# Performance work log

Hardware: AMD Instinct MI355X
Metric: run time of the kernel (lower is better)

## Reference

```python
import jax, jax.numpy as jnp
import numpy as np

N_NODES = 50000
N_EDGES = 800000
SIZES = [128, 256, 256, 128]
EPS = 1e-5


def setup_inputs() -> dict:
    key = jax.random.key(0)
    ks = jax.random.split(key, 2 + 5 * (len(SIZES) - 1))
    inp = {
        "x": jax.random.normal(ks[0], (N_NODES, SIZES[0]), dtype=jnp.float32),
        "edge_index": jax.random.randint(ks[1], (2, N_EDGES), 0, N_NODES, dtype=jnp.int64),
    }
    k = 2
    for i, (fin, fout) in enumerate(zip(SIZES[:-1], SIZES[1:])):
        scale = 1.0 / np.sqrt(fin)
        inp[f"W{i}"] = jax.random.normal(ks[k], (fout, fin), dtype=jnp.float32) * scale; k += 1
        inp[f"b{i}"] = jnp.zeros((fout,), dtype=jnp.float32)
        inp[f"g{i}"] = jnp.ones((fout,), dtype=jnp.float32)   # LayerNorm weight
        inp[f"be{i}"] = jnp.zeros((fout,), dtype=jnp.float32)  # LayerNorm bias
        inp[f"a{i}"] = jnp.full((1,), 0.25, dtype=jnp.float32)  # PReLU slope
        k += 3  # keep key consumption deterministic
    return inp


def _gcn_conv(x, src, dst, dinv, W, b):
    # GCNConv: h = x @ W^T; aggregate norm(src,dst) * h[src] into dst; add bias.
    h = x @ W.T  # [N, F_out]
    norm = dinv[src] * dinv[dst]  # [E+N]
    msg = norm[:, None] * h[src]  # [E+N, F_out]
    return jax.ops.segment_sum(msg, dst, num_segments=N_NODES) + b


def _layernorm_graph(x, g, be):
    # PyG LayerNorm(mode='graph'): normalize over all nodes and channels.
    mu = x.mean()
    xc = x - mu
    var = (xc * xc).mean()
    return xc / jnp.sqrt(var + EPS) * g + be


def _prelu(x, a):
    return jnp.where(x >= 0, x, a * x)


def reference(x, edge_index, W0, b0, g0, be0, a0, W1, b1, g1, be1, a1, W2, b2, g2, be2, a2):
    loop = jnp.arange(N_NODES, dtype=edge_index.dtype)
    src = jnp.concatenate([edge_index[0], loop])  # add self-loops
    dst = jnp.concatenate([edge_index[1], loop])
    deg = jax.ops.segment_sum(jnp.ones_like(dst, dtype=x.dtype), dst, num_segments=N_NODES)
    dinv = jax.lax.rsqrt(deg)  # deg >= 1 due to self-loops
    params = [(W0, b0, g0, be0, a0), (W1, b1, g1, be1, a1), (W2, b2, g2, be2, a2)]
    for W, b, g, be, a in params:
        x = _gcn_conv(x, src, dst, dinv, W, b)
        x = _layernorm_graph(x, g, be)
        x = _prelu(x, a)
    return x
```

## Files before the change

kernel.cpp:

```cpp
#include <hip/hip_runtime.h>

#define N_NODES 50000
#define N_EDGES 800000
#define EPS 1e-5f

typedef __attribute__((ext_vector_type(8))) short bf16x8;
typedef __attribute__((ext_vector_type(4))) float f32x4;
typedef __attribute__((ext_vector_type(4))) unsigned short us4;

__device__ __forceinline__ unsigned short f2b(float f) {
    union { float f; unsigned int u; } v; v.f = f;
    unsigned int r = v.u + 0x7fffu + ((v.u >> 16) & 1u);
    return (unsigned short)(r >> 16);
}
__device__ __forceinline__ float b2f(unsigned short b) {
    union { unsigned int u; float f; } v; v.u = ((unsigned int)b) << 16;
    return v.f;
}

#define RED_BUCKETS 64
#define RED_FLOATS_PER_LAYER (RED_BUCKETS * 16)


#define CV_NX (N_NODES * 128 / 4)
#define CV_N0 (256 * 128 / 4)
#define CV_N1 (256 * 256 / 4)
#define CV_N2 (128 * 256 / 4)

__global__ void prep_kernel(const float* __restrict__ x0, const float* __restrict__ W0,
                            const float* __restrict__ W1, const float* __restrict__ W2,
                            unsigned short* __restrict__ xb, unsigned short* __restrict__ wb0,
                            unsigned short* __restrict__ wb1, unsigned short* __restrict__ wb2,
                            int* __restrict__ deg, int* __restrict__ fill,
                            float* __restrict__ red) {
    int i = blockIdx.x * 256 + threadIdx.x;
    if (i < N_NODES) { deg[i] = 0; fill[i] = 0; }
    if (i < 3 * RED_FLOATS_PER_LAYER) red[i] = 0.f;
    const float* s;
    unsigned short* d;
    int j = i;
    if (j < CV_NX) { s = x0; d = xb; }
    else if ((j -= CV_NX) < CV_N0) { s = W0; d = wb0; }
    else if ((j -= CV_N0) < CV_N1) { s = W1; d = wb1; }
    else if ((j -= CV_N1) < CV_N2) { s = W2; d = wb2; }
    else return;
    float4 v = reinterpret_cast<const float4*>(s)[j];
    us4 o;
    o[0] = f2b(v.x); o[1] = f2b(v.y); o[2] = f2b(v.z); o[3] = f2b(v.w);
    reinterpret_cast<us4*>(d)[j] = o;
}


__global__ void count_kernel(const int* __restrict__ dst, int* __restrict__ deg, int e) {
    for (int i = blockIdx.x * blockDim.x + threadIdx.x; i < e; i += gridDim.x * blockDim.x)
        atomicAdd(&deg[dst[i]], 1);
}

__global__ void scan1_kernel(const int* __restrict__ deg, float* __restrict__ dinv,
                             int* __restrict__ bsum, int n) {
    int i = blockIdx.x * 256 + threadIdx.x;
    int v = (i < n) ? deg[i] : 0;
    if (i < n) dinv[i] = rsqrtf((float)(v + 1));
    int t = v;
    #pragma unroll
    for (int off = 1; off < 64; off <<= 1) t += __shfl_xor(t, off);
    __shared__ int wsum[4];
    int wid = threadIdx.x >> 6, lane = threadIdx.x & 63;
    if (lane == 0) wsum[wid] = t;
    __syncthreads();
    if (threadIdx.x == 0) bsum[blockIdx.x] = wsum[0] + wsum[1] + wsum[2] + wsum[3];
}

__global__ void scan2_kernel(const int* __restrict__ bsum, int* __restrict__ bpre, int nb) {
    __shared__ int sm[256];
    int t = threadIdx.x;
    sm[t] = (t < nb) ? bsum[t] : 0;
    __syncthreads();
    #pragma unroll
    for (int d = 1; d < 256; d <<= 1) {
        int x = (t >= d) ? sm[t - d] : 0;
        __syncthreads();
        sm[t] += x;
        __syncthreads();
    }
    bpre[t] = (t > 0) ? sm[t - 1] : 0;
}

__global__ void scan3_kernel(const int* __restrict__ deg, const int* __restrict__ bpre,
                             int* __restrict__ off, int n) {
    __shared__ int sm[256];
    int t = threadIdx.x;
    int i = blockIdx.x * 256 + t;
    int v = (i < n) ? deg[i] : 0;
    sm[t] = v;
    __syncthreads();
    #pragma unroll
    for (int d = 1; d < 256; d <<= 1) {
        int x = (t >= d) ? sm[t - d] : 0;
        __syncthreads();
        sm[t] += x;
        __syncthreads();
    }
    if (i < n) off[i + 1] = sm[t] + bpre[blockIdx.x];
    if (i == 0) off[0] = 0;
}

__global__ void scatter_kernel(const int* __restrict__ src, const int* __restrict__ dst,
                               const int* __restrict__ coff, int* __restrict__ fill,
                               const float* __restrict__ dinv,
                               unsigned int* __restrict__ epack, int e) {
    for (int i = blockIdx.x * blockDim.x + threadIdx.x; i < e; i += gridDim.x * blockDim.x) {
        int d = dst[i];
        int s = src[i];
        int pos = coff[d] + atomicAdd(&fill[d], 1);
        epack[pos] = ((unsigned int)f2b(dinv[s] * dinv[d]) << 16) | (unsigned int)s;
    }
}


template<int BN, bool TRANSFORM, bool ADD_BIAS, bool FUSE_RED>
__device__ __forceinline__ void gemm_body(
    const unsigned short* __restrict__ Xin, const unsigned short* __restrict__ Wb,
    const float* __restrict__ bias, const float* __restrict__ redin,
    const float* __restrict__ gw, const float* __restrict__ bw,
    const float* __restrict__ asl, float* __restrict__ redout,
    unsigned short* __restrict__ Hout, int M, int K, float inv_count) {
    constexpr int FR_N = BN / 64;
    __shared__ unsigned short xs[2][64 * 32];
    int tid = threadIdx.x;
    int wid = tid >> 6, lane = tid & 63;
    int l16 = lane & 15, kg = lane >> 4;
    int srow = tid >> 2, sblk = tid & 3;
    int m0 = blockIdx.x * 64;
    int colbase = wid * (BN / 4);

    float mu = 0.f, rstd = 0.f, alpha = 0.f;
    if (TRANSFORM) {
        float s = redin[lane * 16], s2 = redin[lane * 16 + 1];
        #pragma unroll
        for (int off = 1; off < 64; off <<= 1) { s += __shfl_xor(s, off); s2 += __shfl_xor(s2, off); }
        mu = s * inv_count;
        rstd = rsqrtf(s2 * inv_count - mu * mu + EPS);
        alpha = asl[0];
    }

    int gm = m0 + srow;
    bool inm = (gm < M);
    const unsigned short* xrow = Xin + (size_t)gm * K + sblk * 8;
    unsigned short* xdst = &xs[0][srow * 32 + ((sblk ^ (srow & 3)) * 8)];

    auto stage = [&](int k0, int buf) {
        bf16x8 xv = {};
        if (inm) {
            bf16x8 u = *reinterpret_cast<const bf16x8*>(xrow + k0);
            if (TRANSFORM) {
                int f0 = k0 + sblk * 8;
                float ga[8], ba[8];
                *reinterpret_cast<float4*>(&ga[0]) = *reinterpret_cast<const float4*>(gw + f0);
                *reinterpret_cast<float4*>(&ga[4]) = *reinterpret_cast<const float4*>(gw + f0 + 4);
                *reinterpret_cast<float4*>(&ba[0]) = *reinterpret_cast<const float4*>(bw + f0);
                *reinterpret_cast<float4*>(&ba[4]) = *reinterpret_cast<const float4*>(bw + f0 + 4);
                #pragma unroll
                for (int i = 0; i < 8; ++i) {
                    float A = rstd * ga[i];
                    float B = ba[i] - mu * A;
                    float v = fmaf(b2f((unsigned short)u[i]), A, B);
                    v = fmaf(fminf(v, 0.f), alpha - 1.0f, v);
                    xv[i] = (short)f2b(v);
                }
            } else {
                xv = u;
            }
        }
        *reinterpret_cast<bf16x8*>(xdst + buf * (64 * 32)) = xv;
    };

    stage(0, 0);
    f32x4 acc[4][FR_N] = {};
    int nsteps = K / 32;
    for (int s = 0; s < nsteps; ++s) {
        __syncthreads();
        int k0 = s * 32;
        if (s + 1 < nsteps) stage(k0 + 32, (s + 1) & 1);
        bf16x8 b[FR_N];
        #pragma unroll
        for (int j = 0; j < FR_N; ++j)
            b[j] = *reinterpret_cast<const bf16x8*>(
                Wb + (size_t)(colbase + j * 16 + l16) * K + k0 + kg * 8);
        const unsigned short* xbuf = xs[s & 1];
        bf16x8 a[4];
        #pragma unroll
        for (int i = 0; i < 4; ++i) {
            int ar = i * 16 + l16;
            a[i] = *reinterpret_cast<const bf16x8*>(xbuf + ar * 32 + ((kg ^ (ar & 3)) * 8));
        }
        #pragma unroll
        for (int i = 0; i < 4; ++i)
            #pragma unroll
            for (int j = 0; j < FR_N; ++j)
                acc[i][j] = __builtin_amdgcn_mfma_f32_16x16x32_bf16(b[j], a[i], acc[i][j], 0, 0, 0);
    }

    float bsel[FR_N][4];
    if (ADD_BIAS) {
        #pragma unroll
        for (int j = 0; j < FR_N; ++j)
            *reinterpret_cast<float4*>(bsel[j]) =
                *reinterpret_cast<const float4*>(bias + colbase + j * 16 + kg * 4);
    }
    float s = 0.f, s2 = 0.f;
    #pragma unroll
    for (int i = 0; i < 4; ++i) {
        int row = m0 + i * 16 + l16;
        if (row < M) {
            #pragma unroll
            for (int j = 0; j < FR_N; ++j) {
                us4 o;
                #pragma unroll
                for (int r = 0; r < 4; ++r) {
                    float v = acc[i][j][r] + (ADD_BIAS ? bsel[j][r] : 0.f);
                    if (FUSE_RED) { s += v; s2 += v * v; }
                    o[r] = f2b(v);
                }
                *reinterpret_cast<us4*>(Hout + (size_t)row * BN + colbase + j * 16 + kg * 4) = o;
            }
        }
    }
    if (FUSE_RED) {
        #pragma unroll
        for (int off = 1; off < 64; off <<= 1) { s += __shfl_xor(s, off); s2 += __shfl_xor(s2, off); }
        if (lane == 0) {
            int bkt = (blockIdx.x & (RED_BUCKETS - 1)) * 16;
            atomicAdd(&redout[bkt], s);
            atomicAdd(&redout[bkt + 1], s2);
        }
    }
}


template<int COLS, bool ADD_BIAS, bool FUSE_RED>
__device__ __forceinline__ void agg_body(
    const unsigned short* __restrict__ Hb, const int* __restrict__ coff,
    const unsigned int* __restrict__ epack, const float* __restrict__ dinv,
    const float* __restrict__ bias, unsigned short* __restrict__ Y,
    float* __restrict__ red) {
    constexpr int RL = COLS / 8;
    constexpr int NG = 64 / RL;
    int node = blockIdx.x * 4 + (threadIdx.x >> 6);
    int lane = threadIdx.x & 63;
    int g = lane / RL;
    int rl = lane % RL;
    float di = dinv[node];
    int s0 = coff[node], s1 = coff[node + 1];
    float acc[8] = {};

    int k = s0 - 1 + g;
    int sc; float wc;
    bf16x8 vc;
    bool have = (k < s1);
    if (have) {
        if (k < s0) { sc = node; wc = di * di; }
        else { unsigned int u = epack[k]; sc = u & 0xffff; wc = b2f((unsigned short)(u >> 16)); }
        vc = *reinterpret_cast<const bf16x8*>(Hb + (size_t)sc * COLS + rl * 8);
    }
    while (have) {
        int k2 = k + NG;
        bool have2 = (k2 < s1);
        int sn = 0; float wn = 0.f;
        bf16x8 vn;
        if (have2) {
            unsigned int u = epack[k2];
            sn = u & 0xffff; wn = b2f((unsigned short)(u >> 16));
            vn = *reinterpret_cast<const bf16x8*>(Hb + (size_t)sn * COLS + rl * 8);
        }
        #pragma unroll
        for (int i = 0; i < 8; ++i) acc[i] += wc * b2f((unsigned short)vc[i]);
        k = k2; wc = wn; vc = vn; have = have2;
    }

    #pragma unroll
    for (int off = RL; off < 64; off <<= 1) {
        #pragma unroll
        for (int i = 0; i < 8; ++i) acc[i] += __shfl_xor(acc[i], off);
    }
    if (ADD_BIAS) {
        #pragma unroll
        for (int i = 0; i < 8; ++i) acc[i] += bias[rl * 8 + i];
    }
    if (FUSE_RED) {
        float s = 0.f, s2 = 0.f;
        if (g == 0) {
            #pragma unroll
            for (int i = 0; i < 8; ++i) { s += acc[i]; s2 += acc[i] * acc[i]; }
        }
        #pragma unroll
        for (int off = 1; off < 64; off <<= 1) { s += __shfl_xor(s, off); s2 += __shfl_xor(s2, off); }
        if (lane == 0) {
            int bkt = (blockIdx.x & (RED_BUCKETS - 1)) * 16;
            atomicAdd(&red[bkt], s);
            atomicAdd(&red[bkt + 1], s2);
        }
    }
    if (g == 0) {
        bf16x8 o;
        #pragma unroll
        for (int i = 0; i < 8; ++i) o[i] = (short)f2b(acc[i]);
        __builtin_nontemporal_store(o, reinterpret_cast<bf16x8*>(Y + (size_t)node * COLS + rl * 8));
    }
}


__global__ __launch_bounds__(256) void gemm_l0(const unsigned short* X, const unsigned short* W,
                                               const float* bias, float* redout,
                                               unsigned short* H, int M, int K, float ic) {
    gemm_body<256, false, true, true>(X, W, bias, nullptr, nullptr, nullptr, nullptr, redout, H, M, K, ic);
}
__global__ __launch_bounds__(256) void gemm_l1(const unsigned short* X, const unsigned short* W,
                                               const float* redin, const float* gw, const float* bw,
                                               const float* asl, unsigned short* H, int M, int K, float ic) {
    gemm_body<256, true, false, false>(X, W, nullptr, redin, gw, bw, asl, nullptr, H, M, K, ic);
}
__global__ __launch_bounds__(256) void gemm_l2(const unsigned short* X, const unsigned short* W,
                                               const float* redin, const float* gw, const float* bw,
                                               const float* asl, unsigned short* H, int M, int K, float ic) {
    gemm_body<128, true, false, false>(X, W, nullptr, redin, gw, bw, asl, nullptr, H, M, K, ic);
}
__global__ void agg_l0(const unsigned short* Hb, const int* coff, const unsigned int* ep,
                       const float* dinv, unsigned short* Y) {
    agg_body<128, false, false>(Hb, coff, ep, dinv, nullptr, Y, nullptr);
}
__global__ void agg_l1(const unsigned short* Hb, const int* coff, const unsigned int* ep,
                       const float* dinv, const float* bias, unsigned short* Y, float* red) {
    agg_body<256, true, true>(Hb, coff, ep, dinv, bias, Y, red);
}
__global__ void agg_l2(const unsigned short* Hb, const int* coff, const unsigned int* ep,
                       const float* dinv, const float* bias, unsigned short* Y, float* red) {
    agg_body<128, true, true>(Hb, coff, ep, dinv, bias, Y, red);
}


__global__ void norm_final(const unsigned short* __restrict__ Yb, const float* __restrict__ red,
                           const float* __restrict__ g, const float* __restrict__ be,
                           const float* __restrict__ a, float* __restrict__ X,
                           int fmask8, int n8, float inv_count) {
    int lane = threadIdx.x & 63;
    float s = red[lane * 16], s2 = red[lane * 16 + 1];
    #pragma unroll
    for (int off = 1; off < 64; off <<= 1) { s += __shfl_xor(s, off); s2 += __shfl_xor(s2, off); }
    float mu = s * inv_count;
    float rstd = rsqrtf(s2 * inv_count - mu * mu + EPS);
    float alpha = a[0];
    for (int i = blockIdx.x * blockDim.x + threadIdx.x; i < n8; i += gridDim.x * blockDim.x) {
        bf16x8 v = reinterpret_cast<const bf16x8*>(Yb)[i];
        int fb = (i & fmask8) * 8;
        float o[8];
        #pragma unroll
        for (int j = 0; j < 8; ++j) {
            float t = (b2f((unsigned short)v[j]) - mu) * rstd * g[fb + j] + be[fb + j];
            o[j] = t >= 0.f ? t : alpha * t;
        }
        float* xp = X + (size_t)i * 8;
        *reinterpret_cast<float4*>(xp) = make_float4(o[0], o[1], o[2], o[3]);
        *reinterpret_cast<float4*>(xp + 4) = make_float4(o[4], o[5], o[6], o[7]);
    }
}


extern "C" void kernel_launch(void* const* d_in, const int* in_sizes, int n_in,
                              void* d_out, int out_size, void* d_ws, size_t ws_size,
                              hipStream_t stream) {
    const float* x0 = (const float*)d_in[0];
    const int* ei = (const int*)d_in[1];
    const float* W[3] = {(const float*)d_in[2], (const float*)d_in[7], (const float*)d_in[12]};
    const float* bb[3] = {(const float*)d_in[3], (const float*)d_in[8], (const float*)d_in[13]};
    const float* gg[3] = {(const float*)d_in[4], (const float*)d_in[9], (const float*)d_in[14]};
    const float* be[3] = {(const float*)d_in[5], (const float*)d_in[10], (const float*)d_in[15]};
    const float* aa[3] = {(const float*)d_in[6], (const float*)d_in[11], (const float*)d_in[16]};

    char* ws = (char*)d_ws;
    size_t o = 0;
    auto alloc = [&](size_t bytes) {
        void* p = ws + o;
        o = (o + bytes + 255) & ~(size_t)255;
        return p;
    };
    int* deg = (int*)alloc(N_NODES * 4);
    int* fill = (int*)alloc(N_NODES * 4);
    int* coff = (int*)alloc((N_NODES + 1) * 4);
    unsigned int* epack = (unsigned int*)alloc((size_t)N_EDGES * 4);
    float* dinv = (float*)alloc(N_NODES * 4);
    int* bsum = (int*)alloc(256 * 4);
    int* bpre = (int*)alloc(256 * 4);
    float* red = (float*)alloc(3 * RED_FLOATS_PER_LAYER * 4);
    unsigned short* Wb0 = (unsigned short*)alloc(256 * 128 * 2);
    unsigned short* Wb1 = (unsigned short*)alloc(256 * 256 * 2);
    unsigned short* Wb2 = (unsigned short*)alloc(128 * 256 * 2);
    unsigned short* xb = (unsigned short*)alloc((size_t)N_NODES * 128 * 2);
    unsigned short* hb = (unsigned short*)alloc((size_t)N_NODES * 256 * 2);
    unsigned short* yb = (unsigned short*)alloc((size_t)N_NODES * 256 * 2);

    const int* e_src = ei;
    const int* e_dst = ei + N_EDGES;
    int nb = (N_NODES + 255) / 256;

    int cvtot = CV_NX + CV_N0 + CV_N1 + CV_N2;
    prep_kernel<<<(cvtot + 255) / 256, 256, 0, stream>>>(x0, W[0], W[1], W[2], xb, Wb0, Wb1, Wb2,
                                                         deg, fill, red);
    count_kernel<<<2048, 256, 0, stream>>>(e_dst, deg, N_EDGES);
    scan1_kernel<<<nb, 256, 0, stream>>>(deg, dinv, bsum, N_NODES);
    scan2_kernel<<<1, 256, 0, stream>>>(bsum, bpre, nb);
    scan3_kernel<<<nb, 256, 0, stream>>>(deg, bpre, coff, N_NODES);
    scatter_kernel<<<2048, 256, 0, stream>>>(e_src, e_dst, coff, fill, dinv, epack, N_EDGES);

    int gm = (N_NODES + 63) / 64;
    float ic256 = 1.0f / (N_NODES * 256.0f);
    float ic128 = 1.0f / (N_NODES * 128.0f);

    agg_l0<<<12500, 256, 0, stream>>>(xb, coff, epack, dinv, hb);
    gemm_l0<<<gm, 256, 0, stream>>>(hb, Wb0, bb[0], red + 0, yb, N_NODES, 128, ic256);

    gemm_l1<<<gm, 256, 0, stream>>>(yb, Wb1, red + 0, gg[0], be[0], aa[0], hb, N_NODES, 256, ic256);
    agg_l1<<<12500, 256, 0, stream>>>(hb, coff, epack, dinv, bb[1], yb, red + RED_FLOATS_PER_LAYER);

    gemm_l2<<<gm, 256, 0, stream>>>(yb, Wb2, red + RED_FLOATS_PER_LAYER, gg[1], be[1], aa[1], hb,
                                    N_NODES, 256, ic256);
    agg_l2<<<12500, 256, 0, stream>>>(hb, coff, epack, dinv, bb[2], yb,
                                      red + 2 * RED_FLOATS_PER_LAYER);

    norm_final<<<2048, 256, 0, stream>>>(yb, red + 2 * RED_FLOATS_PER_LAYER, gg[2], be[2], aa[2],
                                         (float*)d_out, 15, N_NODES * 128 / 8, ic128);
}
```

Measured before the change: 341.1 us.

## Store node features in 32-column chunked layout and aggregate per chunk

Node feature buffers now use a column-chunked layout: each 32-feature slice of all nodes is stored contiguously, so one gathered row segment is 64 bytes. The aggregation kernel changes to match. Each block handles one chunk for 64 nodes, and each node's edge list is walked serially by 4 lanes, with no cross-lane shuffle reduction. The intent is a smaller gather working set per chunk, for better L2 hit rates on the random neighbor reads. In exchange, load balancing across lanes now depends on node degree, and the GEMM and final-normalisation kernels need extra index arithmetic and strided stores.

```diff
diff --git a/kernel.cpp b/kernel.cpp
--- a/kernel.cpp
+++ b/kernel.cpp
@@ -17,6 +17,7 @@
     union { unsigned int u; float f; } v; v.u = ((unsigned int)b) << 16;
     return v.f;
 }
+
 
 #define RED_BUCKETS 64
 #define RED_FLOATS_PER_LAYER (RED_BUCKETS * 16)
@@ -36,11 +37,19 @@
     int i = blockIdx.x * 256 + threadIdx.x;
     if (i < N_NODES) { deg[i] = 0; fill[i] = 0; }
     if (i < 3 * RED_FLOATS_PER_LAYER) red[i] = 0.f;
+    int j = i;
+    if (j < CV_NX) {
+        float4 v = reinterpret_cast<const float4*>(x0)[j];
+        int n = j >> 5;
+        int col0 = (j & 31) * 4;
+        us4 o;
+        o[0] = f2b(v.x); o[1] = f2b(v.y); o[2] = f2b(v.z); o[3] = f2b(v.w);
+        *reinterpret_cast<us4*>(xb + ((size_t)(col0 >> 5) * N_NODES + n) * 32 + (col0 & 31)) = o;
+        return;
+    }
     const float* s;
     unsigned short* d;
-    int j = i;
-    if (j < CV_NX) { s = x0; d = xb; }
-    else if ((j -= CV_NX) < CV_N0) { s = W0; d = wb0; }
+    if ((j -= CV_NX) < CV_N0) { s = W0; d = wb0; }
     else if ((j -= CV_N0) < CV_N1) { s = W1; d = wb1; }
     else if ((j -= CV_N1) < CV_N2) { s = W2; d = wb2; }
     else return;
@@ -144,15 +153,15 @@
         alpha = asl[0];
     }
 
-    int gm = m0 + srow;
-    bool inm = (gm < M);
-    const unsigned short* xrow = Xin + (size_t)gm * K + sblk * 8;
+    int gmr = m0 + srow;
+    bool inm = (gmr < M);
+    const unsigned short* xrow = Xin + (size_t)gmr * 32 + sblk * 8;
     unsigned short* xdst = &xs[0][srow * 32 + ((sblk ^ (srow & 3)) * 8)];
 
     auto stage = [&](int k0, int buf) {
         bf16x8 xv = {};
         if (inm) {
-            bf16x8 u = *reinterpret_cast<const bf16x8*>(xrow + k0);
+            bf16x8 u = *reinterpret_cast<const bf16x8*>(xrow + (size_t)(k0 >> 5) * N_NODES * 32);
             if (TRANSFORM) {
                 int f0 = k0 + sblk * 8;
                 float ga[8], ba[8];
@@ -215,6 +224,7 @@
         if (row < M) {
             #pragma unroll
             for (int j = 0; j < FR_N; ++j) {
+                int col = colbase + j * 16 + kg * 4;
                 us4 o;
                 #pragma unroll
                 for (int r = 0; r < 4; ++r) {
@@ -222,7 +232,8 @@
                     if (FUSE_RED) { s += v; s2 += v * v; }
                     o[r] = f2b(v);
                 }
-                *reinterpret_cast<us4*>(Hout + (size_t)row * BN + colbase + j * 16 + kg * 4) = o;
+                *reinterpret_cast<us4*>(
+                    Hout + ((size_t)(col >> 5) * N_NODES + row) * 32 + (col & 31)) = o;
             }
         }
     }
@@ -244,68 +255,64 @@
     const unsigned int* __restrict__ epack, const float* __restrict__ dinv,
     const float* __restrict__ bias, unsigned short* __restrict__ Y,
     float* __restrict__ red) {
-    constexpr int RL = COLS / 8;
-    constexpr int NG = 64 / RL;
-    int node = blockIdx.x * 4 + (threadIdx.x >> 6);
-    int lane = threadIdx.x & 63;
-    int g = lane / RL;
-    int rl = lane % RL;
-    float di = dinv[node];
-    int s0 = coff[node], s1 = coff[node + 1];
+    constexpr int CHUNKS = COLS / 32;
+    int chunk = blockIdx.x % CHUNKS;
+    int nodeblk = blockIdx.x / CHUNKS;
+    int t = threadIdx.x;
+    int node = nodeblk * 64 + (t >> 2);
+    int rl = t & 3;
+    bool active = node < N_NODES;
+    const unsigned short* base = Hb + (size_t)chunk * N_NODES * 32 + rl * 8;
+    int s0 = 0, s1 = 0;
+    float wc = 0.f;
+    if (active) {
+        s0 = coff[node]; s1 = coff[node + 1];
+        float di = dinv[node];
+        wc = di * di;
+    }
     float acc[8] = {};
-
-    int k = s0 - 1 + g;
-    int sc; float wc;
-    bf16x8 vc;
-    bool have = (k < s1);
-    if (have) {
-        if (k < s0) { sc = node; wc = di * di; }
-        else { unsigned int u = epack[k]; sc = u & 0xffff; wc = b2f((unsigned short)(u >> 16)); }
-        vc = *reinterpret_cast<const bf16x8*>(Hb + (size_t)sc * COLS + rl * 8);
-    }
-    while (have) {
-        int k2 = k + NG;
-        bool have2 = (k2 < s1);
-        int sn = 0; float wn = 0.f;
-        bf16x8 vn;
+    int k = s0 - 1;
+    bf16x8 vc = {};
+    bool have = active;
+    if (have) vc = *reinterpret_cast<const bf16x8*>(base + (size_t)node * 32);
+    while (__any(have)) {
+        int k2 = k + 1;
+        bool have2 = have && (k2 < s1);
+        float wn = 0.f;
+        bf16x8 vn = {};
         if (have2) {
             unsigned int u = epack[k2];
-            sn = u & 0xffff; wn = b2f((unsigned short)(u >> 16));
-            vn = *reinterpret_cast<const bf16x8*>(Hb + (size_t)sn * COLS + rl * 8);
-        }
-        #pragma unroll
-        for (int i = 0; i < 8; ++i) acc[i] += wc * b2f((unsigned short)vc[i]);
+            wn = b2f((unsigned short)(u >> 16));
+            vn = *reinterpret_cast<const bf16x8*>(base + (size_t)(u & 0xffffu) * 32);
+        }
+        if (have) {
+            #pragma unroll
+            for (int i = 0; i < 8; ++i) acc[i] += wc * b2f((unsigned short)vc[i]);
+        }
         k = k2; wc = wn; vc = vn; have = have2;
     }
-
-    #pragma unroll
-    for (int off = RL; off < 64; off <<= 1) {
-        #pragma unroll
-        for (int i = 0; i < 8; ++i) acc[i] += __shfl_xor(acc[i], off);
-    }
-    if (ADD_BIAS) {
-        #pragma unroll
-        for (int i = 0; i < 8; ++i) acc[i] += bias[rl * 8 + i];
+    if (ADD_BIAS && active) {
+        #pragma unroll
+        for (int i = 0; i < 8; ++i) acc[i] += bias[chunk * 32 + rl * 8 + i];
     }
     if (FUSE_RED) {
         float s = 0.f, s2 = 0.f;
-        if (g == 0) {
-            #pragma unroll
-            for (int i = 0; i < 8; ++i) { s += acc[i]; s2 += acc[i] * acc[i]; }
-        }
+        #pragma unroll
+        for (int i = 0; i < 8; ++i) { s += acc[i]; s2 += acc[i] * acc[i]; }
         #pragma unroll
         for (int off = 1; off < 64; off <<= 1) { s += __shfl_xor(s, off); s2 += __shfl_xor(s2, off); }
-        if (lane == 0) {
+        if ((t & 63) == 0) {
             int bkt = (blockIdx.x & (RED_BUCKETS - 1)) * 16;
             atomicAdd(&red[bkt], s);
             atomicAdd(&red[bkt + 1], s2);
         }
     }
-    if (g == 0) {
+    if (active) {
         bf16x8 o;
         #pragma unroll
         for (int i = 0; i < 8; ++i) o[i] = (short)f2b(acc[i]);
-        __builtin_nontemporal_store(o, reinterpret_cast<bf16x8*>(Y + (size_t)node * COLS + rl * 8));
+        __builtin_nontemporal_store(
+            o, reinterpret_cast<bf16x8*>(Y + ((size_t)chunk * N_NODES + node) * 32 + rl * 8));
     }
 }
 
@@ -342,7 +349,7 @@
 __global__ void norm_final(const unsigned short* __restrict__ Yb, const float* __restrict__ red,
                            const float* __restrict__ g, const float* __restrict__ be,
                            const float* __restrict__ a, float* __restrict__ X,
-                           int fmask8, int n8, float inv_count) {
+                           float inv_count) {
     int lane = threadIdx.x & 63;
     float s = red[lane * 16], s2 = red[lane * 16 + 1];
     #pragma unroll
@@ -350,16 +357,21 @@
     float mu = s * inv_count;
     float rstd = rsqrtf(s2 * inv_count - mu * mu + EPS);
     float alpha = a[0];
-    for (int i = blockIdx.x * blockDim.x + threadIdx.x; i < n8; i += gridDim.x * blockDim.x) {
+    int total = N_NODES * 128 / 8;
+    for (int i = blockIdx.x * blockDim.x + threadIdx.x; i < total; i += gridDim.x * blockDim.x) {
         bf16x8 v = reinterpret_cast<const bf16x8*>(Yb)[i];
-        int fb = (i & fmask8) * 8;
+        int c = i / (N_NODES * 4);
+        int rem = i - c * (N_NODES * 4);
+        int n = rem >> 2;
+        int r = rem & 3;
+        int f0 = c * 32 + r * 8;
         float o[8];
         #pragma unroll
         for (int j = 0; j < 8; ++j) {
-            float t = (b2f((unsigned short)v[j]) - mu) * rstd * g[fb + j] + be[fb + j];
+            float t = (b2f((unsigned short)v[j]) - mu) * rstd * g[f0 + j] + be[f0 + j];
             o[j] = t >= 0.f ? t : alpha * t;
         }
-        float* xp = X + (size_t)i * 8;
+        float* xp = X + (size_t)n * 128 + f0;
         *reinterpret_cast<float4*>(xp) = make_float4(o[0], o[1], o[2], o[3]);
         *reinterpret_cast<float4*>(xp + 4) = make_float4(o[4], o[5], o[6], o[7]);
     }
@@ -416,17 +428,17 @@
     float ic256 = 1.0f / (N_NODES * 256.0f);
     float ic128 = 1.0f / (N_NODES * 128.0f);
 
-    agg_l0<<<12500, 256, 0, stream>>>(xb, coff, epack, dinv, hb);
+    agg_l0<<<gm * 4, 256, 0, stream>>>(xb, coff, epack, dinv, hb);
     gemm_l0<<<gm, 256, 0, stream>>>(hb, Wb0, bb[0], red + 0, yb, N_NODES, 128, ic256);
 
     gemm_l1<<<gm, 256, 0, stream>>>(yb, Wb1, red + 0, gg[0], be[0], aa[0], hb, N_NODES, 256, ic256);
-    agg_l1<<<12500, 256, 0, stream>>>(hb, coff, epack, dinv, bb[1], yb, red + RED_FLOATS_PER_LAYER);
+    agg_l1<<<gm * 8, 256, 0, stream>>>(hb, coff, epack, dinv, bb[1], yb, red + RED_FLOATS_PER_LAYER);
 
     gemm_l2<<<gm, 256, 0, stream>>>(yb, Wb2, red + RED_FLOATS_PER_LAYER, gg[1], be[1], aa[1], hb,
                                     N_NODES, 256, ic256);
-    agg_l2<<<12500, 256, 0, stream>>>(hb, coff, epack, dinv, bb[2], yb,
-                                      red + 2 * RED_FLOATS_PER_LAYER);
+    agg_l2<<<gm * 4, 256, 0, stream>>>(hb, coff, epack, dinv, bb[2], yb,
+                                       red + 2 * RED_FLOATS_PER_LAYER);
 
     norm_final<<<2048, 256, 0, stream>>>(yb, red + 2 * RED_FLOATS_PER_LAYER, gg[2], be[2], aa[2],
-                                         (float*)d_out, 15, N_NODES * 128 / 8, ic128);
-}
+                                         (float*)d_out, ic128);
+}
```

Result: faster. 328.6 us (-3.7%).
